# Performance work log

Hardware: AMD Instinct MI355X
Metric: run time of the kernel (lower is better)

## Reference

```python
import jax, jax.numpy as jnp
import numpy as np

N = 50000
E = 800000
F_IN = 128
HID = 16
HEADS = 8
C = 16
NEG_SLOPE = 0.2


def setup_inputs() -> dict:
    key = jax.random.key(0)
    ks = jax.random.split(key, 12)
    glorot = lambda k, shape: jax.random.normal(k, shape, jnp.float32) * jnp.sqrt(2.0 / (shape[0] + shape[-1]))
    return {
        "x": jax.random.normal(ks[0], (N, F_IN), jnp.float32),
        "edge_index": jax.random.randint(ks[1], (2, E), 0, N, jnp.int32),
        "x2": jax.random.normal(ks[2], (N, F_IN), jnp.float32),
        "edge_index2": jax.random.randint(ks[3], (2, E), 0, N, jnp.int32),
        # conv1: GATConv(F_IN -> HID, heads=HEADS, concat=True)
        "W1": glorot(ks[4], (F_IN, HEADS * HID)),
        "a1_src": glorot(ks[5], (HEADS, HID)),
        "a1_dst": glorot(ks[6], (HEADS, HID)),
        "b1": jnp.zeros((HEADS * HID,), jnp.float32),
        # conv2: GATConv(HEADS*HID -> C, heads=1, concat=False)
        "W2": glorot(ks[7], (HEADS * HID, 1 * C)),
        "a2_src": glorot(ks[8], (1, C)),
        "a2_dst": glorot(ks[9], (1, C)),
        "b2": jnp.zeros((C,), jnp.float32),
    }


def gat_conv(x, edge_index, W, a_src, a_dst, bias, concat):
    """PyG-style GATConv with self-loops, segment softmax over destinations."""
    n = x.shape[0]
    heads, out = a_src.shape
    h = (x @ W).reshape(n, heads, out)               # [N, H, O]
    loops = jnp.arange(n, dtype=edge_index.dtype)
    src = jnp.concatenate([edge_index[0], loops])     # messages flow src -> dst
    dst = jnp.concatenate([edge_index[1], loops])
    alpha_s = jnp.einsum('nho,ho->nh', h, a_src)
    alpha_d = jnp.einsum('nho,ho->nh', h, a_dst)
    e = jax.nn.leaky_relu(alpha_s[src] + alpha_d[dst], NEG_SLOPE)  # [E+N, H]
    m = jax.lax.stop_gradient(jax.ops.segment_max(e, dst, num_segments=n))
    w = jnp.exp(e - m[dst])
    denom = jax.ops.segment_sum(w, dst, num_segments=n)
    alpha = w / (denom[dst] + 1e-16)                  # segment softmax
    msg = h[src] * alpha[:, :, None]                  # [E+N, H, O]
    agg = jax.ops.segment_sum(msg, dst, num_segments=n)
    agg = agg.reshape(n, heads * out) if concat else agg.mean(axis=1)
    return agg + bias


def forward_once(x, edge_index, W1, a1_src, a1_dst, b1, W2, a2_src, a2_dst, b2):
    # dropout(p=0.6) is identity in eval mode
    h = jax.nn.elu(gat_conv(x, edge_index, W1, a1_src, a1_dst, b1, concat=True))
    return gat_conv(h, edge_index, W2, a2_src, a2_dst, b2, concat=False)


def reference(x, edge_index, x2, edge_index2, W1, a1_src, a1_dst, b1, W2, a2_src, a2_dst, b2):
    y = forward_once(x, edge_index, W1, a1_src, a1_dst, b1, W2, a2_src, a2_dst, b2)
    z = forward_once(x2, edge_index2, W1, a1_src, a1_dst, b1, W2, a2_src, a2_dst, b2)
    eps = 1e-8
    ny = jnp.maximum(jnp.linalg.norm(y, axis=1), eps)
    nz = jnp.maximum(jnp.linalg.norm(z, axis=1), eps)
    cos = jnp.sum(y * z, axis=1) / (ny * nz)
    ls_y = jax.nn.log_softmax(y, axis=1)
    ls_z = jax.nn.log_softmax(z, axis=1)
    return (ls_y, 1.0 - cos, ls_z, ls_y, ls_y)
```

## Files before the change

kernel.cpp:

```cpp
#include <hip/hip_runtime.h>
#include <hip/hip_bf16.h>

#define N_NODES 50000
#define N_EDGES 800000
#define F_INS   128
#define HIDDEN  16
#define HEADS   8
#define HO      128
#define C_OUT   16
#define NEG_SLOPE 0.2f
#define SLOT    64
#define NB_G1   ((N_NODES + 63) / 64)
#define NB_GAT1 ((N_NODES + 3) / 4)
#define NB_G2   ((N_NODES + 16) / 16)

#define NP      50016
#define AS_ST   ((size_t)NP * 8)
#define H1B_ST  ((size_t)NP * 64)
#define HL1_ST  ((size_t)N_NODES * 64)
#define H2_ST   ((size_t)NP * 16)
#define AS2_ST  ((size_t)NP)

#define NCLS     128
#define CLS_MUL  1342u
#define CLS_SH   19
#define CAP      8192
#define CHUNK    2048
#define NB_BKT   ((N_EDGES + CHUNK - 1) / CHUNK)

typedef unsigned short u16;
typedef unsigned int   u32;
typedef int v4i __attribute__((ext_vector_type(4)));
typedef short bf16x8 __attribute__((ext_vector_type(8)));
typedef float f32x4 __attribute__((ext_vector_type(4)));

__device__ __forceinline__ float bf2f(u16 u) {
    union { u32 i; float f; } t; t.i = ((u32)u) << 16; return t.f;
}
__device__ __forceinline__ float bflo(u32 q) {
    union { u32 i; float f; } t; t.i = q << 16; return t.f;
}
__device__ __forceinline__ float bfhi(u32 q) {
    union { u32 i; float f; } t; t.i = q & 0xFFFF0000u; return t.f;
}
__device__ __forceinline__ u32 f2bf(float f) {
    union { float f; u32 i; } t; t.f = f;
    u32 x = t.i;
    u32 lsb = (x >> 16) & 1u;
    x += 0x7FFFu + lsb;
    return x >> 16;
}
__device__ __forceinline__ u32 cvtpk(float lo, float hi) {
    u32 r;
    asm("v_cvt_pk_bf16_f32 %0, %1, %2" : "=v"(r) : "v"(lo), "v"(hi));
    return r;
}
__device__ __forceinline__ float lrelu(float t) {
    return fmaxf(t, NEG_SLOPE * t);
}
__device__ __forceinline__ int cls_of(int d) { return (int)(((u32)d * CLS_MUL) >> CLS_SH); }
__host__ __device__ __forceinline__ int cls_base(int c) { return (int)(((u32)c * 524288u + (CLS_MUL - 1)) / CLS_MUL); }

__global__ void k_wt(const float* __restrict__ W1, const float* __restrict__ a1s,
                     const float* __restrict__ a1d, u32* __restrict__ w1t,
                     u32* __restrict__ a1t) {
    int t = threadIdx.x;
    if (blockIdx.x < 32) {
        int e = blockIdx.x * 256 + t;
        int c = e >> 6, kp = e & 63;
        float lo = W1[(2 * kp) * 128 + c];
        float hi = W1[(2 * kp + 1) * 128 + c];
        w1t[e] = (f2bf(hi) << 16) | f2bf(lo);
    } else {
        #pragma unroll
        for (int i = 0; i < 4; ++i) {
            int wi = t + i * 256;
            int n = wi >> 6, kp = wi & 63;
            int h = n >> 1;
            const float* av = ((n & 1) ? a1d : a1s) + h * 16;
            float s0 = 0.f, s1 = 0.f;
            #pragma unroll
            for (int c = 0; c < 16; ++c) {
                s0 += W1[(2 * kp) * 128 + h * 16 + c] * av[c];
                s1 += W1[(2 * kp + 1) * 128 + h * 16 + c] * av[c];
            }
            a1t[wi] = (f2bf(s1) << 16) | f2bf(s0);
        }
    }
}

__launch_bounds__(256)
__global__ void k_bucket(const int* __restrict__ ei0, const int* __restrict__ ei1,
                         int* __restrict__ gcur, u32* __restrict__ bucket) {
    __shared__ int cnt[NCLS];
    __shared__ int base[NCLS];
    int t = threadIdx.x;
    int g = blockIdx.x & 1;
    int chunk = blockIdx.x >> 1;
    int e0 = chunk * CHUNK + t * 8;
    bool act = e0 < N_EDGES;

    if (t < NCLS) cnt[t] = 0;
    __syncthreads();

    const int* src = g ? ei1 : ei0;
    const int* dst = src + N_EDGES;
    int d8[8], s8[8], c8[8];
    if (act) {
        v4i da = *(const v4i*)(dst + e0), db = *(const v4i*)(dst + e0 + 4);
        v4i sa = *(const v4i*)(src + e0), sb = *(const v4i*)(src + e0 + 4);
        d8[0]=da[0]; d8[1]=da[1]; d8[2]=da[2]; d8[3]=da[3];
        d8[4]=db[0]; d8[5]=db[1]; d8[6]=db[2]; d8[7]=db[3];
        s8[0]=sa[0]; s8[1]=sa[1]; s8[2]=sa[2]; s8[3]=sa[3];
        s8[4]=sb[0]; s8[5]=sb[1]; s8[6]=sb[2]; s8[7]=sb[3];
        #pragma unroll
        for (int j = 0; j < 8; ++j) {
            c8[j] = cls_of(d8[j]);
            atomicAdd(&cnt[c8[j]], 1);
        }
    }
    __syncthreads();
    if (t < NCLS) {
        int n = cnt[t];
        base[t] = n ? atomicAdd(&gcur[g * NCLS + t], n) : 0;
        cnt[t] = 0;
    }
    __syncthreads();
    if (act) {
        #pragma unroll
        for (int j = 0; j < 8; ++j) {
            int c = c8[j];
            int p = atomicAdd(&cnt[c], 1);
            bucket[(size_t)(g * NCLS + c) * CAP + base[c] + p] =
                ((u32)d8[j] << 16) | (u32)s8[j];
        }
    }
}

__launch_bounds__(256)
__global__ void k_build(const int* __restrict__ gcur, const u32* __restrict__ bucket,
                        int* __restrict__ cursor, u16* __restrict__ col) {
    __shared__ int cnt[391];
    __shared__ __align__(16) u16 scol[391 * SLOT];
    int t = threadIdx.x;
    int c = blockIdx.x & (NCLS - 1);
    int g = blockIdx.x >> 7;
    int d0 = cls_base(c);
    int d1 = (c == NCLS - 1) ? N_NODES : cls_base(c + 1);
    int nn = d1 - d0;
    for (int j = t; j < nn; j += 256) cnt[j] = 0;
    __syncthreads();

    int size = gcur[g * NCLS + c];
    const u32* bp = bucket + (size_t)(g * NCLS + c) * CAP;
    for (int i = t; i < size; i += 256) {
        u32 e = bp[i];
        int d = (int)(e >> 16);
        int s = (int)(e & 0xFFFFu);
        int p = atomicAdd(&cnt[d - d0], 1);
        if (p < SLOT) scol[(d - d0) * SLOT + p] = (u16)s;
    }
    __syncthreads();
    int* cur = cursor + g * N_NODES;
    for (int j = t; j < nn; j += 256) {
        int raw = cnt[j];
        int n0 = min(raw, SLOT);
        int n1 = (n0 + 7) & ~7;
        for (int p = n0; p < n1; ++p) scol[j * SLOT + p] = (u16)N_NODES;
        cur[d0 + j] = raw;
    }
    __syncthreads();
    uint4* dst = (uint4*)(col + ((size_t)g * N_NODES + d0) * SLOT);
    const uint4* srcv = (const uint4*)scol;
    int n16 = nn * 8;
    for (int i = t; i < n16; i += 256) dst[i] = srcv[i];
}

__launch_bounds__(256)
__global__ void k_gemm1(const float* __restrict__ x1g, const float* __restrict__ x2g,
                        const u32* __restrict__ w1t, const u32* __restrict__ a1t,
                        u32* __restrict__ h1b, float* __restrict__ as_,
                        float* __restrict__ ad_) {
    __shared__ u32 xls[4096];
    int t = threadIdx.x;
    int bid = blockIdx.x;
    int g = bid >= NB_G1;
    if (g) bid -= NB_G1;
    const float* x = g ? x2g : x1g;
    u32*   h1o = h1b + (size_t)g * H1B_ST;
    float* aso = as_ + (size_t)g * AS_ST;
    float* ado = ad_ + (size_t)g * AS_ST;
    int r0 = bid * 64;

    const float2* x2p = (const float2*)x;
    #pragma unroll
    for (int i = 0; i < 16; ++i) {
        int A = t + i * 256;
        int wi = A >> 10, kt = (A >> 8) & 3, L = (A >> 2) & 63, jj = A & 3;
        int m = L & 15, qd = L >> 4;
        int r = r0 + wi * 16 + m;
        int pp = kt * 16 + qd * 4 + jj;
        float2 v = make_float2(0.f, 0.f);
        if (r < N_NODES) v = x2p[(size_t)r * 64 + pp];
        xls[A] = cvtpk(v.x, v.y);
    }
    __syncthreads();

    int lane = t & 63;
    int wid = t >> 6;
    int n = lane & 15, quad = lane >> 4;

    f32x4 acc[8], acca;
    #pragma unroll
    for (int ct = 0; ct < 8; ++ct) acc[ct] = (f32x4){0.f, 0.f, 0.f, 0.f};
    acca = (f32x4){0.f, 0.f, 0.f, 0.f};

    #pragma unroll
    for (int kt = 0; kt < 4; ++kt) {
        union { uint4 u; bf16x8 v; } af;
        af.u = *(const uint4*)(xls + wid * 1024 + kt * 256 + lane * 4);
        #pragma unroll
        for (int ct = 0; ct < 8; ++ct) {
            union { uint4 u; bf16x8 v; } bf_;
            bf_.u = *(const uint4*)(w1t + (ct * 16 + n) * 64 + kt * 16 + quad * 4);
            acc[ct] = __builtin_amdgcn_mfma_f32_16x16x32_bf16(af.v, bf_.v, acc[ct], 0, 0, 0);
        }
        union { uint4 u; bf16x8 v; } ba;
        ba.u = *(const uint4*)(a1t + n * 64 + kt * 16 + quad * 4);
        acca = __builtin_amdgcn_mfma_f32_16x16x32_bf16(af.v, ba.v, acca, 0, 0, 0);
    }

    int h = n >> 1;
    #pragma unroll
    for (int reg = 0; reg < 4; ++reg) {
        int gr = r0 + wid * 16 + quad * 4 + reg;
        bool ok = gr <= N_NODES;
        float av = (gr == N_NODES) ? -1e30f : acca[reg];
        if (ok) {
            if (n & 1) ado[gr * 8 + h] = av;
            else       aso[gr * 8 + h] = av;
        }
        #pragma unroll
        for (int ct = 0; ct < 8; ++ct) {
            float ot = __shfl_xor(acc[ct][reg], 1);
            if (!(n & 1) && ok)
                h1o[(size_t)gr * 64 + ct * 8 + (n >> 1)] = cvtpk(acc[ct][reg], ot);
        }
    }
}

#define GAT1_ISSUE(I, q0,q1,q2,q3,q4,q5,q6,q7, A) do { \
    u32 ix_=(I).x, iy_=(I).y, iz_=(I).z, iw_=(I).w; \
    q0 = *(const u32*)(h1c + (((ix_ & 0xFFFFu) << 8) | lane4)); \
    q1 = *(const u32*)(h1c + (((ix_ >> 16)     << 8) | lane4)); \
    q2 = *(const u32*)(h1c + (((iy_ & 0xFFFFu) << 8) | lane4)); \
    q3 = *(const u32*)(h1c + (((iy_ >> 16)     << 8) | lane4)); \
    q4 = *(const u32*)(h1c + (((iz_ & 0xFFFFu) << 8) | lane4)); \
    q5 = *(const u32*)(h1c + (((iz_ >> 16)     << 8) | lane4)); \
    q6 = *(const u32*)(h1c + (((iw_ & 0xFFFFu) << 8) | lane4)); \
    q7 = *(const u32*)(h1c + (((iw_ >> 16)     << 8) | lane4)); \
    u32 ds_ = (j8 & 4) ? ((j8 & 2) ? iw_ : iz_) : ((j8 & 2) ? iy_ : ix_); \
    u32 sA_ = (j8 & 1) ? (ds_ >> 16) : (ds_ & 0xFFFFu); \
    A = *(const float*)(asc + ((sA_ << 5) | ha4)); \
} while (0)

#define GAT1_CONS(q0,q1,q2,q3,q4,q5,q6,q7, A) do { \
    int wli_ = __float_as_int(__expf(lrelu((A) + ad_a))); \
    float w0 = __int_as_float(__builtin_amdgcn_ds_bpermute(vb,       wli_)); \
    float w1 = __int_as_float(__builtin_amdgcn_ds_bpermute(vb + 32,  wli_)); \
    float w2 = __int_as_float(__builtin_amdgcn_ds_bpermute(vb + 64,  wli_)); \
    float w3 = __int_as_float(__builtin_amdgcn_ds_bpermute(vb + 96,  wli_)); \
    float w4 = __int_as_float(__builtin_amdgcn_ds_bpermute(vb + 128, wli_)); \
    float w5 = __int_as_float(__builtin_amdgcn_ds_bpermute(vb + 160, wli_)); \
    float w6 = __int_as_float(__builtin_amdgcn_ds_bpermute(vb + 192, wli_)); \
    float w7 = __int_as_float(__builtin_amdgcn_ds_bpermute(vb + 224, wli_)); \
    denom += ((w0 + w1) + (w2 + w3)) + ((w4 + w5) + (w6 + w7)); \
    ax += w0 * bflo(q0) + w1 * bflo(q1) + w2 * bflo(q2) + w3 * bflo(q3) \
        + w4 * bflo(q4) + w5 * bflo(q5) + w6 * bflo(q6) + w7 * bflo(q7); \
    ay += w0 * bfhi(q0) + w1 * bfhi(q1) + w2 * bfhi(q2) + w3 * bfhi(q3) \
        + w4 * bfhi(q4) + w5 * bfhi(q5) + w6 * bfhi(q6) + w7 * bfhi(q7); \
} while (0)

__launch_bounds__(256)
__global__ void k_gat1(const u32* __restrict__ h1b, const float* __restrict__ as_,
                       const float* __restrict__ ad_, const int* __restrict__ cursor,
                       const u16* __restrict__ col, const float* __restrict__ b1,
                       u32* __restrict__ hL1) {
    int t = threadIdx.x;
    int lane = t & 63;
    int bid = blockIdx.x;
    int g = bid >= NB_GAT1;
    if (g) bid -= NB_GAT1;
    int node = bid * 4 + (t >> 6);

    const char*  h1c = (const char*)(h1b + (size_t)g * H1B_ST);
    const char*  asc = (const char*)(as_ + (size_t)g * AS_ST);
    const float* ad1 = ad_ + (size_t)g * AS_ST;
    const u16*   cp  = col + ((size_t)g * N_NODES + node) * SLOT;

    int hc = lane >> 3;
    int ha = lane & 7;
    int j8 = lane >> 3;
    int vb = hc << 2;
    u32 lane4 = (u32)lane << 2;
    u32 ha4 = (u32)ha << 2;

    float ad_a = ad1[node * 8 + ha];
    float as_c = as_[(size_t)g * AS_ST + node * 8 + hc];
    float ad_c = ad1[node * 8 + hc];

    float w = __expf(lrelu(as_c + ad_c));
    float denom = w;
    u32 q = *(const u32*)(h1c + (((u32)node << 8) | lane4));
    float ax = w * bflo(q), ay = w * bfhi(q);

    int deg = min(cursor[g * N_NODES + node], SLOT);
    int nb = (deg + 7) >> 3;
    if (nb) {
        u32 qa0,qa1,qa2,qa3,qa4,qa5,qa6,qa7;
        u32 qb0,qb1,qb2,qb3,qb4,qb5,qb6,qb7;
        float Aa, Ab;
        uint4 Ia, Ib;
        Ia = *(const uint4*)cp;
        GAT1_ISSUE(Ia, qa0,qa1,qa2,qa3,qa4,qa5,qa6,qa7, Aa);
        if (nb > 1) {
            Ib = *(const uint4*)(cp + 8);
            GAT1_ISSUE(Ib, qb0,qb1,qb2,qb3,qb4,qb5,qb6,qb7, Ab);
        }
        int b = 0;
        for (;;) {
            GAT1_CONS(qa0,qa1,qa2,qa3,qa4,qa5,qa6,qa7, Aa);
            if (++b >= nb) break;
            if (b + 1 < nb) {
                Ia = *(const uint4*)(cp + (b + 1) * 8);
                GAT1_ISSUE(Ia, qa0,qa1,qa2,qa3,qa4,qa5,qa6,qa7, Aa);
            }
            GAT1_CONS(qb0,qb1,qb2,qb3,qb4,qb5,qb6,qb7, Ab);
            if (++b >= nb) break;
            if (b + 1 < nb) {
                Ib = *(const uint4*)(cp + (b + 1) * 8);
                GAT1_ISSUE(Ib, qb0,qb1,qb2,qb3,qb4,qb5,qb6,qb7, Ab);
            }
        }
    }
    float inv = 1.f / (denom + 1e-16f);
    int c = lane * 2;
    float o0 = ax * inv + b1[c];
    float o1 = ay * inv + b1[c + 1];
    o0 = (o0 > 0.f) ? o0 : (__expf(o0) - 1.f);
    o1 = (o1 > 0.f) ? o1 : (__expf(o1) - 1.f);
    hL1[(size_t)g * HL1_ST + (size_t)node * 64 + lane] = cvtpk(o0, o1);
}

__launch_bounds__(256)
__global__ void k_gemm2(const u32* __restrict__ hL1, const float* __restrict__ W2,
                        const float* __restrict__ a2s, const float* __restrict__ a2d,
                        float* __restrict__ h2, float* __restrict__ as2,
                        float* __restrict__ ad2) {
    __shared__ float w2s[F_INS * C_OUT];
    __shared__ float hs[16 * 136];
    int t = threadIdx.x;
    int bid = blockIdx.x;
    int g = bid >= NB_G2;
    if (g) bid -= NB_G2;
    const u16* hL = (const u16*)(hL1 + (size_t)g * HL1_ST);
    float* h2o  = h2  + (size_t)g * H2_ST;
    float* as2o = as2 + (size_t)g * AS2_ST;
    float* ad2o = ad2 + (size_t)g * AS2_ST;

    const float4* w4 = (const float4*)W2;
    #pragma unroll
    for (int i = 0; i < 2; ++i) {
        int idx = t + i * 256;
        ((float4*)w2s)[idx] = w4[idx];
    }
    int r0 = bid * 16;
    const ushort4* hg = (const ushort4*)hL;
    #pragma unroll
    for (int i = 0; i < 2; ++i) {
        int idx = t + i * 256;
        int r  = idx >> 5;
        int c4 = idx & 31;
        ushort4 qq = make_ushort4(0, 0, 0, 0);
        if (r0 + r < N_NODES) qq = hg[(size_t)(r0 + r) * 32 + c4];
        float4 v; v.x = bf2f(qq.x); v.y = bf2f(qq.y); v.z = bf2f(qq.z); v.w = bf2f(qq.w);
        *(float4*)(hs + r * 136 + c4 * 4) = v;
    }
    __syncthreads();

    int c = t & 15, r = t >> 4;
    float acc = 0.f;
    #pragma unroll 8
    for (int k = 0; k < F_INS; ++k) acc += hs[r * 136 + k] * w2s[k * C_OUT + c];
    int n = r0 + r;
    if (n <= N_NODES) h2o[(size_t)n * C_OUT + c] = acc;

    float sa = acc * a2s[c];
    float sd = acc * a2d[c];
    #pragma unroll
    for (int m = 1; m < 16; m <<= 1) {
        sa += __shfl_xor(sa, m);
        sd += __shfl_xor(sd, m);
    }
    if (c == 0 && n <= N_NODES) {
        as2o[n] = (n == N_NODES) ? -1e30f : sa;
        ad2o[n] = sd;
    }
}

#define GAT2_ISSUE(I, v0,v1,v2,v3,v4,v5,v6,v7, A) do { \
    u32 ix_=(I).x, iy_=(I).y, iz_=(I).z, iw_=(I).w; \
    v0 = *(const float*)(h2c + (((ix_ & 0xFFFFu) << 6) | c4)); \
    v1 = *(const float*)(h2c + (((ix_ >> 16)     << 6) | c4)); \
    v2 = *(const float*)(h2c + (((iy_ & 0xFFFFu) << 6) | c4)); \
    v3 = *(const float*)(h2c + (((iy_ >> 16)     << 6) | c4)); \
    v4 = *(const float*)(h2c + (((iz_ & 0xFFFFu) << 6) | c4)); \
    v5 = *(const float*)(h2c + (((iz_ >> 16)     << 6) | c4)); \
    v6 = *(const float*)(h2c + (((iw_ & 0xFFFFu) << 6) | c4)); \
    v7 = *(const float*)(h2c + (((iw_ >> 16)     << 6) | c4)); \
    u32 ds_ = (jsel & 4) ? ((jsel & 2) ? iw_ : iz_) : ((jsel & 2) ? iy_ : ix_); \
    u32 sA_ = (jsel & 1) ? (ds_ >> 16) : (ds_ & 0xFFFFu); \
    A = *(const float*)(as2c + (sA_ << 2)); \
} while (0)

#define GAT2_CONS(v0,v1,v2,v3,v4,v5,v6,v7, A) do { \
    int wli_ = __float_as_int(__expf(lrelu((A) + ad))); \
    float w0 = __int_as_float(__builtin_amdgcn_ds_bpermute(gb,      wli_)); \
    float w1 = __int_as_float(__builtin_amdgcn_ds_bpermute(gb + 4,  wli_)); \
    float w2 = __int_as_float(__builtin_amdgcn_ds_bpermute(gb + 8,  wli_)); \
    float w3 = __int_as_float(__builtin_amdgcn_ds_bpermute(gb + 12, wli_)); \
    float w4 = __int_as_float(__builtin_amdgcn_ds_bpermute(gb + 16, wli_)); \
    float w5 = __int_as_float(__builtin_amdgcn_ds_bpermute(gb + 20, wli_)); \
    float w6 = __int_as_float(__builtin_amdgcn_ds_bpermute(gb + 24, wli_)); \
    float w7 = __int_as_float(__builtin_amdgcn_ds_bpermute(gb + 28, wli_)); \
    denom += ((w0 + w1) + (w2 + w3)) + ((w4 + w5) + (w6 + w7)); \
    acc += (w0 * v0 + w1 * v1 + w2 * v2 + w3 * v3) \
         + (w4 * v4 + w5 * v5 + w6 * v6 + w7 * v7); \
} while (0)

__device__ __forceinline__ float gat2_node(const char* h2c, const char* as2c,
                                           const float* __restrict__ ad2g, int deg,
                                           const u16* __restrict__ cp, int node,
                                           u32 c4, int jsel, u32 gb, float b2c) {
    float ad = ad2g[node];
    float w = __expf(lrelu(*(const float*)(as2c + ((u32)node << 2)) + ad));
    float denom = w;
    float acc = w * *(const float*)(h2c + (((u32)node << 6) | c4));

    int nb = (deg + 7) >> 3;
    if (nb) {
        float va0,va1,va2,va3,va4,va5,va6,va7;
        float vc0,vc1,vc2,vc3,vc4,vc5,vc6,vc7;
        float Aa, Ac;
        uint4 Ia, Ic;
        Ia = *(const uint4*)cp;
        GAT2_ISSUE(Ia, va0,va1,va2,va3,va4,va5,va6,va7, Aa);
        if (nb > 1) {
            Ic = *(const uint4*)(cp + 8);
            GAT2_ISSUE(Ic, vc0,vc1,vc2,vc3,vc4,vc5,vc6,vc7, Ac);
        }
        int b = 0;
        for (;;) {
            GAT2_CONS(va0,va1,va2,va3,va4,va5,va6,va7, Aa);
            if (++b >= nb) break;
            if (b + 1 < nb) {
                Ia = *(const uint4*)(cp + (b + 1) * 8);
                GAT2_ISSUE(Ia, va0,va1,va2,va3,va4,va5,va6,va7, Aa);
            }
            GAT2_CONS(vc0,vc1,vc2,vc3,vc4,vc5,vc6,vc7, Ac);
            if (++b >= nb) break;
            if (b + 1 < nb) {
                Ic = *(const uint4*)(cp + (b + 1) * 8);
                GAT2_ISSUE(Ic, vc0,vc1,vc2,vc3,vc4,vc5,vc6,vc7, Ac);
            }
        }
    }
    return acc / (denom + 1e-16f) + b2c;
}

__launch_bounds__(256)
__global__ void k_gat2e(const float* __restrict__ h2, const float* __restrict__ as2,
                        const float* __restrict__ ad2, const int* __restrict__ cursor,
                        const u16* __restrict__ col, const float* __restrict__ b2,
                        float* __restrict__ out) {
    int t = threadIdx.x;
    int node = blockIdx.x * 16 + (t >> 4);
    int c = t & 15;
    int lane = t & 63;
    u32 c4 = (u32)c << 2;
    int jsel = lane & 7;
    u32 gb = (u32)(lane & 48) << 2;
    float b2c = b2[c];

    int degY = min(cursor[node], SLOT);
    int degZ = min(cursor[N_NODES + node], SLOT);
    float yv = gat2_node((const char*)h2, (const char*)as2, ad2, degY,
                         col + (size_t)node * SLOT, node, c4, jsel, gb, b2c);
    float zv = gat2_node((const char*)(h2 + H2_ST), (const char*)(as2 + AS2_ST),
                         ad2 + AS2_ST, degZ,
                         col + ((size_t)N_NODES + node) * SLOT, node, c4, jsel, gb, b2c);

    float my = yv, mz = zv;
    #pragma unroll
    for (int m = 1; m < 16; m <<= 1) {
        my = fmaxf(my, __shfl_xor(my, m));
        mz = fmaxf(mz, __shfl_xor(mz, m));
    }
    float sy = __expf(yv - my), sz = __expf(zv - mz);
    float dot = yv * zv, ny = yv * yv, nz = zv * zv;
    #pragma unroll
    for (int m = 1; m < 16; m <<= 1) {
        sy  += __shfl_xor(sy, m);
        sz  += __shfl_xor(sz, m);
        dot += __shfl_xor(dot, m);
        ny  += __shfl_xor(ny, m);
        nz  += __shfl_xor(nz, m);
    }
    float lsey = my + __logf(sy);
    float lsez = mz + __logf(sz);
    float omc = 1.f - dot / (fmaxf(sqrtf(ny), 1e-8f) * fmaxf(sqrtf(nz), 1e-8f));

    const int O1 = N_NODES * C_OUT;
    const int O2 = O1 + N_NODES;
    const int O3 = O2 + N_NODES * C_OUT;
    const int O4 = O3 + N_NODES * C_OUT;
    float ly = yv - lsey;
    float lz = zv - lsez;
    int base = node * 16 + c;
    out[base]      = ly;
    out[O2 + base] = lz;
    out[O3 + base] = ly;
    out[O4 + base] = ly;
    if (c == 0) out[O1 + node] = omc;
}

extern "C" void kernel_launch(void* const* d_in, const int* in_sizes, int n_in,
                              void* d_out, int out_size, void* d_ws, size_t ws_size,
                              hipStream_t stream) {
    (void)in_sizes; (void)n_in; (void)out_size; (void)ws_size;
    const float* x1  = (const float*)d_in[0];
    const int*   ei1 = (const int*)d_in[1];
    const float* x2  = (const float*)d_in[2];
    const int*   ei2 = (const int*)d_in[3];
    const float* W1  = (const float*)d_in[4];
    const float* a1s = (const float*)d_in[5];
    const float* a1d = (const float*)d_in[6];
    const float* b1  = (const float*)d_in[7];
    const float* W2  = (const float*)d_in[8];
    const float* a2s = (const float*)d_in[9];
    const float* a2d = (const float*)d_in[10];
    const float* b2  = (const float*)d_in[11];
    float* out = (float*)d_out;

    char* p = (char*)d_ws;
    int* gcur      = (int*)p; p += (size_t)2 * NCLS * 4;
    u32* w1t       = (u32*)p; p += (size_t)128 * 64 * 4;
    u32* a1t       = (u32*)p; p += (size_t)16 * 64 * 4;
    int* cursor    = (int*)p; p += (size_t)2 * N_NODES * 4;
    u16* col       = (u16*)p; p += (size_t)2 * N_NODES * SLOT * 2;
    float* as1  = (float*)p; p += (size_t)2 * AS_ST * 4;
    float* ad1  = (float*)p; p += (size_t)2 * AS_ST * 4;
    float* h2   = (float*)p; p += (size_t)2 * H2_ST * 4;
    float* as2  = (float*)p; p += (size_t)2 * AS2_ST * 4;
    float* ad2  = (float*)p; p += (size_t)2 * AS2_ST * 4;
    u32* hL1    = (u32*)p;   p += (size_t)2 * HL1_ST * 4;
    u32* h1b    = (u32*)p;   p += (size_t)2 * H1B_ST * 4;
    u32* bucket = h1b;

    hipMemsetAsync(gcur, 0, (size_t)2 * NCLS * 4, stream);
    k_wt    <<<33, 256, 0, stream>>>(W1, a1s, a1d, w1t, a1t);
    k_bucket<<<2 * NB_BKT, 256, 0, stream>>>(ei1, ei2, gcur, bucket);
    k_build <<<2 * NCLS, 256, 0, stream>>>(gcur, bucket, cursor, col);
    k_gemm1 <<<2 * NB_G1, 256, 0, stream>>>(x1, x2, w1t, a1t, h1b, as1, ad1);
    k_gat1  <<<2 * NB_GAT1, 256, 0, stream>>>(h1b, as1, ad1, cursor, col, b1, hL1);
    k_gemm2 <<<2 * NB_G2, 256, 0, stream>>>(hL1, W2, a2s, a2d, h2, as2, ad2);
    k_gat2e <<<N_NODES / 16, 256, 0, stream>>>(h2, as2, ad2, cursor, col, b2, out);
}
```

Measured before the change: 315.6 us.

## Merge bucketing and GEMM1 into one launch, interleave Y/Z gathers in GAT2

Edge bucketing and the first GEMM now share one launch (k_bg1), with block-index ranges choosing the work, so the independent phases run concurrently and a launch is dropped. The gcur memset is folded into k_wt, and the bucket scratch moves from h1b to hL1 so it no longer aliases the GEMM output written in the same launch. k_gat2e interleaves the Y and Z graph aggregations in one loop so both gather streams are in flight together. In exchange, register pressure rises in gat2e and LDS use in the fused kernel grows, which may lower occupancy.

```diff
diff --git a/kernel.cpp b/kernel.cpp
--- a/kernel.cpp
+++ b/kernel.cpp
@@ -63,7 +63,7 @@
 
 __global__ void k_wt(const float* __restrict__ W1, const float* __restrict__ a1s,
                      const float* __restrict__ a1d, u32* __restrict__ w1t,
-                     u32* __restrict__ a1t) {
+                     u32* __restrict__ a1t, int* __restrict__ gcur) {
     int t = threadIdx.x;
     if (blockIdx.x < 32) {
         int e = blockIdx.x * 256 + t;
@@ -72,6 +72,7 @@
         float hi = W1[(2 * kp + 1) * 128 + c];
         w1t[e] = (f2bf(hi) << 16) | f2bf(lo);
     } else {
+        gcur[t] = 0;
         #pragma unroll
         for (int i = 0; i < 4; ++i) {
             int wi = t + i * 256;
@@ -90,49 +91,123 @@
 }
 
 __launch_bounds__(256)
-__global__ void k_bucket(const int* __restrict__ ei0, const int* __restrict__ ei1,
-                         int* __restrict__ gcur, u32* __restrict__ bucket) {
+__global__ void k_bg1(const int* __restrict__ ei0, const int* __restrict__ ei1,
+                      int* __restrict__ gcur, u32* __restrict__ bucket,
+                      const float* __restrict__ x1g, const float* __restrict__ x2g,
+                      const u32* __restrict__ w1t, const u32* __restrict__ a1t,
+                      u32* __restrict__ h1b, float* __restrict__ as_,
+                      float* __restrict__ ad_) {
+    __shared__ u32 xls[4096];
     __shared__ int cnt[NCLS];
-    __shared__ int base[NCLS];
+    __shared__ int bse[NCLS];
     int t = threadIdx.x;
-    int g = blockIdx.x & 1;
-    int chunk = blockIdx.x >> 1;
-    int e0 = chunk * CHUNK + t * 8;
-    bool act = e0 < N_EDGES;
-
-    if (t < NCLS) cnt[t] = 0;
+
+    if (blockIdx.x < 2 * NB_BKT) {
+        int g = blockIdx.x & 1;
+        int chunk = blockIdx.x >> 1;
+        int e0 = chunk * CHUNK + t * 8;
+        bool act = e0 < N_EDGES;
+
+        if (t < NCLS) cnt[t] = 0;
+        __syncthreads();
+
+        const int* src = g ? ei1 : ei0;
+        const int* dst = src + N_EDGES;
+        int d8[8], s8[8], c8[8];
+        if (act) {
+            v4i da = *(const v4i*)(dst + e0), db = *(const v4i*)(dst + e0 + 4);
+            v4i sa = *(const v4i*)(src + e0), sb = *(const v4i*)(src + e0 + 4);
+            d8[0]=da[0]; d8[1]=da[1]; d8[2]=da[2]; d8[3]=da[3];
+            d8[4]=db[0]; d8[5]=db[1]; d8[6]=db[2]; d8[7]=db[3];
+            s8[0]=sa[0]; s8[1]=sa[1]; s8[2]=sa[2]; s8[3]=sa[3];
+            s8[4]=sb[0]; s8[5]=sb[1]; s8[6]=sb[2]; s8[7]=sb[3];
+            #pragma unroll
+            for (int j = 0; j < 8; ++j) {
+                c8[j] = cls_of(d8[j]);
+                atomicAdd(&cnt[c8[j]], 1);
+            }
+        }
+        __syncthreads();
+        if (t < NCLS) {
+            int n = cnt[t];
+            bse[t] = n ? atomicAdd(&gcur[g * NCLS + t], n) : 0;
+            cnt[t] = 0;
+        }
+        __syncthreads();
+        if (act) {
+            #pragma unroll
+            for (int j = 0; j < 8; ++j) {
+                int c = c8[j];
+                int p = atomicAdd(&cnt[c], 1);
+                bucket[(size_t)(g * NCLS + c) * CAP + bse[c] + p] =
+                    ((u32)d8[j] << 16) | (u32)s8[j];
+            }
+        }
+        return;
+    }
+
+    int bid = blockIdx.x - 2 * NB_BKT;
+    int g = bid >= NB_G1;
+    if (g) bid -= NB_G1;
+    const float* x = g ? x2g : x1g;
+    u32*   h1o = h1b + (size_t)g * H1B_ST;
+    float* aso = as_ + (size_t)g * AS_ST;
+    float* ado = ad_ + (size_t)g * AS_ST;
+    int r0 = bid * 64;
+
+    const float2* x2p = (const float2*)x;
+    #pragma unroll
+    for (int i = 0; i < 16; ++i) {
+        int A = t + i * 256;
+        int wi = A >> 10, kt = (A >> 8) & 3, L = (A >> 2) & 63, jj = A & 3;
+        int m = L & 15, qd = L >> 4;
+        int r = r0 + wi * 16 + m;
+        int pp = kt * 16 + qd * 4 + jj;
+        float2 v = make_float2(0.f, 0.f);
+        if (r < N_NODES) v = x2p[(size_t)r * 64 + pp];
+        xls[A] = cvtpk(v.x, v.y);
+    }
     __syncthreads();
 
-    const int* src = g ? ei1 : ei0;
-    const int* dst = src + N_EDGES;
-    int d8[8], s8[8], c8[8];
-    if (act) {
-        v4i da = *(const v4i*)(dst + e0), db = *(const v4i*)(dst + e0 + 4);
-        v4i sa = *(const v4i*)(src + e0), sb = *(const v4i*)(src + e0 + 4);
-        d8[0]=da[0]; d8[1]=da[1]; d8[2]=da[2]; d8[3]=da[3];
-        d8[4]=db[0]; d8[5]=db[1]; d8[6]=db[2]; d8[7]=db[3];
-        s8[0]=sa[0]; s8[1]=sa[1]; s8[2]=sa[2]; s8[3]=sa[3];
-        s8[4]=sb[0]; s8[5]=sb[1]; s8[6]=sb[2]; s8[7]=sb[3];
+    int lane = t & 63;
+    int wid = t >> 6;
+    int n = lane & 15, quad = lane >> 4;
+
+    f32x4 acc[8], acca;
+    #pragma unroll
+    for (int ct = 0; ct < 8; ++ct) acc[ct] = (f32x4){0.f, 0.f, 0.f, 0.f};
+    acca = (f32x4){0.f, 0.f, 0.f, 0.f};
+
+    #pragma unroll
+    for (int kt = 0; kt < 4; ++kt) {
+        union { uint4 u; bf16x8 v; } af;
+        af.u = *(const uint4*)(xls + wid * 1024 + kt * 256 + lane * 4);
         #pragma unroll
-        for (int j = 0; j < 8; ++j) {
-            c8[j] = cls_of(d8[j]);
-            atomicAdd(&cnt[c8[j]], 1);
-        }
-    }
-    __syncthreads();
-    if (t < NCLS) {
-        int n = cnt[t];
-        base[t] = n ? atomicAdd(&gcur[g * NCLS + t], n) : 0;
-        cnt[t] = 0;
-    }
-    __syncthreads();
-    if (act) {
+        for (int ct = 0; ct < 8; ++ct) {
+            union { uint4 u; bf16x8 v; } bf_;
+            bf_.u = *(const uint4*)(w1t + (ct * 16 + n) * 64 + kt * 16 + quad * 4);
+            acc[ct] = __builtin_amdgcn_mfma_f32_16x16x32_bf16(af.v, bf_.v, acc[ct], 0, 0, 0);
+        }
+        union { uint4 u; bf16x8 v; } ba;
+        ba.u = *(const uint4*)(a1t + n * 64 + kt * 16 + quad * 4);
+        acca = __builtin_amdgcn_mfma_f32_16x16x32_bf16(af.v, ba.v, acca, 0, 0, 0);
+    }
+
+    int h = n >> 1;
+    #pragma unroll
+    for (int reg = 0; reg < 4; ++reg) {
+        int gr = r0 + wid * 16 + quad * 4 + reg;
+        bool ok = gr <= N_NODES;
+        float av = (gr == N_NODES) ? -1e30f : acca[reg];
+        if (ok) {
+            if (n & 1) ado[gr * 8 + h] = av;
+            else       aso[gr * 8 + h] = av;
+        }
         #pragma unroll
-        for (int j = 0; j < 8; ++j) {
-            int c = c8[j];
-            int p = atomicAdd(&cnt[c], 1);
-            bucket[(size_t)(g * NCLS + c) * CAP + base[c] + p] =
-                ((u32)d8[j] << 16) | (u32)s8[j];
+        for (int ct = 0; ct < 8; ++ct) {
+            float ot = __shfl_xor(acc[ct][reg], 1);
+            if (!(n & 1) && ok)
+                h1o[(size_t)gr * 64 + ct * 8 + (n >> 1)] = cvtpk(acc[ct][reg], ot);
         }
     }
 }
@@ -174,79 +249,6 @@
     const uint4* srcv = (const uint4*)scol;
     int n16 = nn * 8;
     for (int i = t; i < n16; i += 256) dst[i] = srcv[i];
-}
-
-__launch_bounds__(256)
-__global__ void k_gemm1(const float* __restrict__ x1g, const float* __restrict__ x2g,
-                        const u32* __restrict__ w1t, const u32* __restrict__ a1t,
-                        u32* __restrict__ h1b, float* __restrict__ as_,
-                        float* __restrict__ ad_) {
-    __shared__ u32 xls[4096];
-    int t = threadIdx.x;
-    int bid = blockIdx.x;
-    int g = bid >= NB_G1;
-    if (g) bid -= NB_G1;
-    const float* x = g ? x2g : x1g;
-    u32*   h1o = h1b + (size_t)g * H1B_ST;
-    float* aso = as_ + (size_t)g * AS_ST;
-    float* ado = ad_ + (size_t)g * AS_ST;
-    int r0 = bid * 64;
-
-    const float2* x2p = (const float2*)x;
-    #pragma unroll
-    for (int i = 0; i < 16; ++i) {
-        int A = t + i * 256;
-        int wi = A >> 10, kt = (A >> 8) & 3, L = (A >> 2) & 63, jj = A & 3;
-        int m = L & 15, qd = L >> 4;
-        int r = r0 + wi * 16 + m;
-        int pp = kt * 16 + qd * 4 + jj;
-        float2 v = make_float2(0.f, 0.f);
-        if (r < N_NODES) v = x2p[(size_t)r * 64 + pp];
-        xls[A] = cvtpk(v.x, v.y);
-    }
-    __syncthreads();
-
-    int lane = t & 63;
-    int wid = t >> 6;
-    int n = lane & 15, quad = lane >> 4;
-
-    f32x4 acc[8], acca;
-    #pragma unroll
-    for (int ct = 0; ct < 8; ++ct) acc[ct] = (f32x4){0.f, 0.f, 0.f, 0.f};
-    acca = (f32x4){0.f, 0.f, 0.f, 0.f};
-
-    #pragma unroll
-    for (int kt = 0; kt < 4; ++kt) {
-        union { uint4 u; bf16x8 v; } af;
-        af.u = *(const uint4*)(xls + wid * 1024 + kt * 256 + lane * 4);
-        #pragma unroll
-        for (int ct = 0; ct < 8; ++ct) {
-            union { uint4 u; bf16x8 v; } bf_;
-            bf_.u = *(const uint4*)(w1t + (ct * 16 + n) * 64 + kt * 16 + quad * 4);
-            acc[ct] = __builtin_amdgcn_mfma_f32_16x16x32_bf16(af.v, bf_.v, acc[ct], 0, 0, 0);
-        }
-        union { uint4 u; bf16x8 v; } ba;
-        ba.u = *(const uint4*)(a1t + n * 64 + kt * 16 + quad * 4);
-        acca = __builtin_amdgcn_mfma_f32_16x16x32_bf16(af.v, ba.v, acca, 0, 0, 0);
-    }
-
-    int h = n >> 1;
-    #pragma unroll
-    for (int reg = 0; reg < 4; ++reg) {
-        int gr = r0 + wid * 16 + quad * 4 + reg;
-        bool ok = gr <= N_NODES;
-        float av = (gr == N_NODES) ? -1e30f : acca[reg];
-        if (ok) {
-            if (n & 1) ado[gr * 8 + h] = av;
-            else       aso[gr * 8 + h] = av;
-        }
-        #pragma unroll
-        for (int ct = 0; ct < 8; ++ct) {
-            float ot = __shfl_xor(acc[ct][reg], 1);
-            if (!(n & 1) && ok)
-                h1o[(size_t)gr * 64 + ct * 8 + (n >> 1)] = cvtpk(acc[ct][reg], ot);
-        }
-    }
 }
 
 #define GAT1_ISSUE(I, q0,q1,q2,q3,q4,q5,q6,q7, A) do { \
@@ -408,23 +410,23 @@
     }
 }
 
-#define GAT2_ISSUE(I, v0,v1,v2,v3,v4,v5,v6,v7, A) do { \
+#define G2_ISSUE(I, H2C, ASC, v0,v1,v2,v3,v4,v5,v6,v7, A) do { \
     u32 ix_=(I).x, iy_=(I).y, iz_=(I).z, iw_=(I).w; \
-    v0 = *(const float*)(h2c + (((ix_ & 0xFFFFu) << 6) | c4)); \
-    v1 = *(const float*)(h2c + (((ix_ >> 16)     << 6) | c4)); \
-    v2 = *(const float*)(h2c + (((iy_ & 0xFFFFu) << 6) | c4)); \
-    v3 = *(const float*)(h2c + (((iy_ >> 16)     << 6) | c4)); \
-    v4 = *(const float*)(h2c + (((iz_ & 0xFFFFu) << 6) | c4)); \
-    v5 = *(const float*)(h2c + (((iz_ >> 16)     << 6) | c4)); \
-    v6 = *(const float*)(h2c + (((iw_ & 0xFFFFu) << 6) | c4)); \
-    v7 = *(const float*)(h2c + (((iw_ >> 16)     << 6) | c4)); \
+    v0 = *(const float*)((H2C) + (((ix_ & 0xFFFFu) << 6) | c4)); \
+    v1 = *(const float*)((H2C) + (((ix_ >> 16)     << 6) | c4)); \
+    v2 = *(const float*)((H2C) + (((iy_ & 0xFFFFu) << 6) | c4)); \
+    v3 = *(const float*)((H2C) + (((iy_ >> 16)     << 6) | c4)); \
+    v4 = *(const float*)((H2C) + (((iz_ & 0xFFFFu) << 6) | c4)); \
+    v5 = *(const float*)((H2C) + (((iz_ >> 16)     << 6) | c4)); \
+    v6 = *(const float*)((H2C) + (((iw_ & 0xFFFFu) << 6) | c4)); \
+    v7 = *(const float*)((H2C) + (((iw_ >> 16)     << 6) | c4)); \
     u32 ds_ = (jsel & 4) ? ((jsel & 2) ? iw_ : iz_) : ((jsel & 2) ? iy_ : ix_); \
     u32 sA_ = (jsel & 1) ? (ds_ >> 16) : (ds_ & 0xFFFFu); \
-    A = *(const float*)(as2c + (sA_ << 2)); \
+    A = *(const float*)((ASC) + (sA_ << 2)); \
 } while (0)
 
-#define GAT2_CONS(v0,v1,v2,v3,v4,v5,v6,v7, A) do { \
-    int wli_ = __float_as_int(__expf(lrelu((A) + ad))); \
+#define G2_CONS(v0,v1,v2,v3,v4,v5,v6,v7, A, AD, DEN, ACC) do { \
+    int wli_ = __float_as_int(__expf(lrelu((A) + (AD)))); \
     float w0 = __int_as_float(__builtin_amdgcn_ds_bpermute(gb,      wli_)); \
     float w1 = __int_as_float(__builtin_amdgcn_ds_bpermute(gb + 4,  wli_)); \
     float w2 = __int_as_float(__builtin_amdgcn_ds_bpermute(gb + 8,  wli_)); \
@@ -433,50 +435,10 @@
     float w5 = __int_as_float(__builtin_amdgcn_ds_bpermute(gb + 20, wli_)); \
     float w6 = __int_as_float(__builtin_amdgcn_ds_bpermute(gb + 24, wli_)); \
     float w7 = __int_as_float(__builtin_amdgcn_ds_bpermute(gb + 28, wli_)); \
-    denom += ((w0 + w1) + (w2 + w3)) + ((w4 + w5) + (w6 + w7)); \
-    acc += (w0 * v0 + w1 * v1 + w2 * v2 + w3 * v3) \
+    DEN += ((w0 + w1) + (w2 + w3)) + ((w4 + w5) + (w6 + w7)); \
+    ACC += (w0 * v0 + w1 * v1 + w2 * v2 + w3 * v3) \
          + (w4 * v4 + w5 * v5 + w6 * v6 + w7 * v7); \
 } while (0)
-
-__device__ __forceinline__ float gat2_node(const char* h2c, const char* as2c,
-                                           const float* __restrict__ ad2g, int deg,
-                                           const u16* __restrict__ cp, int node,
-                                           u32 c4, int jsel, u32 gb, float b2c) {
-    float ad = ad2g[node];
-    float w = __expf(lrelu(*(const float*)(as2c + ((u32)node << 2)) + ad));
-    float denom = w;
-    float acc = w * *(const float*)(h2c + (((u32)node << 6) | c4));
-
-    int nb = (deg + 7) >> 3;
-    if (nb) {
-        float va0,va1,va2,va3,va4,va5,va6,va7;
-        float vc0,vc1,vc2,vc3,vc4,vc5,vc6,vc7;
-        float Aa, Ac;
-        uint4 Ia, Ic;
-        Ia = *(const uint4*)cp;
-        GAT2_ISSUE(Ia, va0,va1,va2,va3,va4,va5,va6,va7, Aa);
-        if (nb > 1) {
-            Ic = *(const uint4*)(cp + 8);
-            GAT2_ISSUE(Ic, vc0,vc1,vc2,vc3,vc4,vc5,vc6,vc7, Ac);
-        }
-        int b = 0;
-        for (;;) {
-            GAT2_CONS(va0,va1,va2,va3,va4,va5,va6,va7, Aa);
-            if (++b >= nb) break;
-            if (b + 1 < nb) {
-                Ia = *(const uint4*)(cp + (b + 1) * 8);
-                GAT2_ISSUE(Ia, va0,va1,va2,va3,va4,va5,va6,va7, Aa);
-            }
-            GAT2_CONS(vc0,vc1,vc2,vc3,vc4,vc5,vc6,vc7, Ac);
-            if (++b >= nb) break;
-            if (b + 1 < nb) {
-                Ic = *(const uint4*)(cp + (b + 1) * 8);
-                GAT2_ISSUE(Ic, vc0,vc1,vc2,vc3,vc4,vc5,vc6,vc7, Ac);
-            }
-        }
-    }
-    return acc / (denom + 1e-16f) + b2c;
-}
 
 __launch_bounds__(256)
 __global__ void k_gat2e(const float* __restrict__ h2, const float* __restrict__ as2,
@@ -492,13 +454,51 @@
     u32 gb = (u32)(lane & 48) << 2;
     float b2c = b2[c];
 
-    int degY = min(cursor[node], SLOT);
-    int degZ = min(cursor[N_NODES + node], SLOT);
-    float yv = gat2_node((const char*)h2, (const char*)as2, ad2, degY,
-                         col + (size_t)node * SLOT, node, c4, jsel, gb, b2c);
-    float zv = gat2_node((const char*)(h2 + H2_ST), (const char*)(as2 + AS2_ST),
-                         ad2 + AS2_ST, degZ,
-                         col + ((size_t)N_NODES + node) * SLOT, node, c4, jsel, gb, b2c);
+    const char* h2Y = (const char*)h2;
+    const char* h2Z = (const char*)(h2 + H2_ST);
+    const char* asY = (const char*)as2;
+    const char* asZ = (const char*)(as2 + AS2_ST);
+    const u16* cpY = col + (size_t)node * SLOT;
+    const u16* cpZ = col + ((size_t)N_NODES + node) * SLOT;
+    float adY = ad2[node];
+    float adZ = ad2[AS2_ST + node];
+
+    float wY = __expf(lrelu(*(const float*)(asY + ((u32)node << 2)) + adY));
+    float dY = wY;
+    float aY = wY * *(const float*)(h2Y + (((u32)node << 6) | c4));
+    float wZ = __expf(lrelu(*(const float*)(asZ + ((u32)node << 2)) + adZ));
+    float dZ = wZ;
+    float aZ = wZ * *(const float*)(h2Z + (((u32)node << 6) | c4));
+
+    int nbY = (min(cursor[node], SLOT) + 7) >> 3;
+    int nbZ = (min(cursor[N_NODES + node], SLOT) + 7) >> 3;
+
+    float y0,y1,y2,y3,y4,y5,y6,y7, Ay;
+    float z0,z1,z2,z3,z4,z5,z6,z7, Az;
+    uint4 I;
+    if (nbY) { I = *(const uint4*)cpY; G2_ISSUE(I, h2Y, asY, y0,y1,y2,y3,y4,y5,y6,y7, Ay); }
+    if (nbZ) { I = *(const uint4*)cpZ; G2_ISSUE(I, h2Z, asZ, z0,z1,z2,z3,z4,z5,z6,z7, Az); }
+    int bY = 0, bZ = 0;
+    while (bY < nbY || bZ < nbZ) {
+        if (bY < nbY) {
+            G2_CONS(y0,y1,y2,y3,y4,y5,y6,y7, Ay, adY, dY, aY);
+            ++bY;
+            if (bY < nbY) {
+                I = *(const uint4*)(cpY + bY * 8);
+                G2_ISSUE(I, h2Y, asY, y0,y1,y2,y3,y4,y5,y6,y7, Ay);
+            }
+        }
+        if (bZ < nbZ) {
+            G2_CONS(z0,z1,z2,z3,z4,z5,z6,z7, Az, adZ, dZ, aZ);
+            ++bZ;
+            if (bZ < nbZ) {
+                I = *(const uint4*)(cpZ + bZ * 8);
+                G2_ISSUE(I, h2Z, asZ, z0,z1,z2,z3,z4,z5,z6,z7, Az);
+            }
+        }
+    }
+    float yv = aY / (dY + 1e-16f) + b2c;
+    float zv = aZ / (dZ + 1e-16f) + b2c;
 
     float my = yv, mz = zv;
     #pragma unroll
@@ -565,13 +565,12 @@
     float* ad2  = (float*)p; p += (size_t)2 * AS2_ST * 4;
     u32* hL1    = (u32*)p;   p += (size_t)2 * HL1_ST * 4;
     u32* h1b    = (u32*)p;   p += (size_t)2 * H1B_ST * 4;
-    u32* bucket = h1b;
-
-    hipMemsetAsync(gcur, 0, (size_t)2 * NCLS * 4, stream);
-    k_wt    <<<33, 256, 0, stream>>>(W1, a1s, a1d, w1t, a1t);
-    k_bucket<<<2 * NB_BKT, 256, 0, stream>>>(ei1, ei2, gcur, bucket);
+    u32* bucket = hL1;
+
+    k_wt    <<<33, 256, 0, stream>>>(W1, a1s, a1d, w1t, a1t, gcur);
+    k_bg1   <<<2 * NB_BKT + 2 * NB_G1, 256, 0, stream>>>(ei1, ei2, gcur, bucket,
+                                                         x1, x2, w1t, a1t, h1b, as1, ad1);
     k_build <<<2 * NCLS, 256, 0, stream>>>(gcur, bucket, cursor, col);
-    k_gemm1 <<<2 * NB_G1, 256, 0, stream>>>(x1, x2, w1t, a1t, h1b, as1, ad1);
     k_gat1  <<<2 * NB_GAT1, 256, 0, stream>>>(h1b, as1, ad1, cursor, col, b1, hL1);
     k_gemm2 <<<2 * NB_G2, 256, 0, stream>>>(hL1, W2, a2s, a2d, h2, as2, ad2);
     k_gat2e <<<N_NODES / 16, 256, 0, stream>>>(h2, as2, ad2, cursor, col, b2, out);
```

Result: no change. 310.9 us (-1.5%).
